# Performance work log

Hardware: AMD Instinct MI355X
Metric: run time of the kernel (lower is better)

Reference implementation:

```python
import jax, jax.numpy as jnp
import numpy as np

TOP_K = 8
ROUTED_SCALING_FACTOR = 1.0
EPS = 1e-20


def setup_inputs() -> dict:
    key = jax.random.key(0)
    k1, k2, k3 = jax.random.split(key, 3)
    T, D, E = 8192, 4096, 64
    x = jax.random.normal(k1, (T, D), dtype=jnp.float32)
    gate_weight = jax.random.normal(k2, (E, D), dtype=jnp.float32) * (1.0 / np.sqrt(D))
    bias = jax.random.normal(k3, (E,), dtype=jnp.float32) * 0.1
    return {"x": x, "gate_weight": gate_weight, "bias": bias}


def reference(x, gate_weight, bias):
    # logits: [T, E] = x [T, D] @ gate_weight.T [D, E]
    logits = jnp.einsum('td,ed->te', x.astype(jnp.float32), gate_weight)
    scores = jax.nn.sigmoid(logits)
    biased = scores + bias  # broadcast [E]
    # top-k on biased scores, sorted descending
    _, indices = jax.lax.top_k(biased, TOP_K)  # [T, K]
    selected_scores = jnp.take_along_axis(scores, indices, axis=-1)  # [T, K]
    normalized = selected_scores / (jnp.sum(selected_scores, axis=-1, keepdims=True) + EPS)
    weights = normalized * ROUTED_SCALING_FACTOR
    return (indices, weights)
```

## Files before the change

kernel.cpp:

```cpp
#include <hip/hip_runtime.h>
#include <math.h>
#include <stdint.h>

#define T_TOK 8192
#define DDIM  4096
#define NEXP  64
#define TOPK  8
#define MT    128
#define BK    32
#define RS    2048.0f

typedef __attribute__((ext_vector_type(8))) _Float16 half8;
typedef __attribute__((ext_vector_type(4))) float f32x4;
typedef __attribute__((address_space(3))) uint32_t lds_u32;
typedef const __attribute__((address_space(1))) uint32_t glb_u32;

__global__ __launch_bounds__(256) void pack_w(
    const float* __restrict__ gw, _Float16* __restrict__ wpk)
{
    const int g    = blockIdx.x * 256 + threadIdx.x;
    const int lane = g & 63;
    const int n    = (g >> 6) & 3;
    const int kt   = g >> 8;
    const int e    = n * 16 + (lane & 15);
    const int k    = kt * 32 + (lane >> 4) * 8;

    const float* src = gw + (size_t)e * DDIM + k;
    float4 v0 = *reinterpret_cast<const float4*>(src);
    float4 v1 = *reinterpret_cast<const float4*>(src + 4);
    const float v[8] = {v0.x, v0.y, v0.z, v0.w, v1.x, v1.y, v1.z, v1.w};

    half8 h0, h1;
    #pragma unroll
    for (int j = 0; j < 8; j++) {
        _Float16 a = (_Float16)v[j];
        h0[j] = a;
        h1[j] = (_Float16)((v[j] - (float)a) * RS);
    }
    _Float16* dst = wpk + (size_t)kt * 4096 + (size_t)(n * 2) * 512 + lane * 8;
    *reinterpret_cast<half8*>(dst)       = h0;
    *reinterpret_cast<half8*>(dst + 512) = h1;
}

template<int STEPS>
__global__ __launch_bounds__(512) void gemm_part(
    const float* __restrict__ x, const _Float16* __restrict__ wpk,
    float* __restrict__ part)
{
    __shared__ float    A[2][MT * BK];
    __shared__ _Float16 B[2][4096];

    const int tid  = threadIdx.x;
    const int lane = tid & 63;
    const int wv   = tid >> 6;
    const int wm   = wv & 3;
    const int wn   = wv >> 2;
    const int mt   = blockIdx.x & 63;
    const int slc  = blockIdx.x >> 6;
    const int m0   = mt * MT;
    const int kt0  = slc * STEPS;
    const int am   = lane & 15;
    const int ag   = lane >> 4;

    const int s_row0 = tid >> 3;
    const int s_c    = tid & 7;

#define STAGE(buf_, t_) do {                                                   \
        const size_t koff = (size_t)(kt0 + (t_)) * BK;                         \
        {                                       \
            int c0 = s_c ^ (s_row0 & 7);                                       \
            __builtin_amdgcn_global_load_lds(                                  \
                (glb_u32*)(x + (size_t)(m0 + s_row0) * DDIM + koff + c0 * 4),  \
                (lds_u32*)(&A[buf_][tid * 4]), 16, 0, 0);                      \
            int r1 = s_row0 + 64;                                              \
            int c1 = s_c ^ (r1 & 7);                                           \
            __builtin_amdgcn_global_load_lds(                                  \
                (glb_u32*)(x + (size_t)(m0 + r1) * DDIM + koff + c1 * 4),      \
                (lds_u32*)(&A[buf_][2048 + tid * 4]), 16, 0, 0);               \
        }                                                                      \
        {                                     \
            const _Float16* bs = wpk + (size_t)(kt0 + (t_)) * 4096 + tid * 8;  \
            __builtin_amdgcn_global_load_lds(                                  \
                (glb_u32*)bs, (lds_u32*)(&B[buf_][tid * 8]), 16, 0, 0);        \
        }                                                                      \
    } while (0)

    f32x4 aH[2][2], aM[2][2];
    #pragma unroll
    for (int f = 0; f < 2; f++)
        #pragma unroll
        for (int n = 0; n < 2; n++) {
            aH[f][n] = (f32x4){0.f, 0.f, 0.f, 0.f};
            aM[f][n] = (f32x4){0.f, 0.f, 0.f, 0.f};
        }

    STAGE(0, 0);
    __syncthreads();

    #pragma unroll 2
    for (int t = 0; t < STEPS; t++) {
        const int buf = t & 1;
        if (t + 1 < STEPS) STAGE(buf ^ 1, t + 1);

        half8 B0[2], B1[2];
        #pragma unroll
        for (int nf = 0; nf < 2; nf++) {
            const int nb = ((wn * 2 + nf) * 2) * 512 + lane * 8;
            B0[nf] = *reinterpret_cast<const half8*>(&B[buf][nb]);
            B1[nf] = *reinterpret_cast<const half8*>(&B[buf][nb + 512]);
        }

        #pragma unroll
        for (int f = 0; f < 2; f++) {
            const int row = wm * 32 + f * 16 + am;
            const int sw  = am & 7;
            float4 alo = *reinterpret_cast<const float4*>(
                &A[buf][row * BK + ((ag * 2 + 0) ^ sw) * 4]);
            float4 ahi = *reinterpret_cast<const float4*>(
                &A[buf][row * BK + ((ag * 2 + 1) ^ sw) * 4]);
            const float vv[8] = {alo.x, alo.y, alo.z, alo.w,
                                 ahi.x, ahi.y, ahi.z, ahi.w};
            half8 a0, a1;
            #pragma unroll
            for (int j = 0; j < 8; j++) {
                float v = vv[j];
                _Float16 h = (_Float16)v;
                a0[j] = h;
                a1[j] = (_Float16)((v - (float)h) * RS);
            }
            #pragma unroll
            for (int nf = 0; nf < 2; nf++) {
                aH[f][nf] = __builtin_amdgcn_mfma_f32_16x16x32_f16(a0, B0[nf], aH[f][nf], 0, 0, 0);
                aM[f][nf] = __builtin_amdgcn_mfma_f32_16x16x32_f16(a0, B1[nf], aM[f][nf], 0, 0, 0);
                aM[f][nf] = __builtin_amdgcn_mfma_f32_16x16x32_f16(a1, B0[nf], aM[f][nf], 0, 0, 0);
            }
        }
        __syncthreads();
    }
#undef STAGE

    const float i1 = 1.0f / RS;
    float* po = part + (size_t)slc * T_TOK * NEXP + (size_t)m0 * NEXP;
    #pragma unroll
    for (int f = 0; f < 2; f++)
        #pragma unroll
        for (int nf = 0; nf < 2; nf++)
            #pragma unroll
            for (int r = 0; r < 4; r++)
                po[(size_t)(wm * 32 + f * 16 + ag * 4 + r) * NEXP
                   + (wn * 2 + nf) * 16 + am]
                    = aH[f][nf][r] + aM[f][nf][r] * i1;
}

__global__ __launch_bounds__(256) void reduce_topk(
    const float* __restrict__ part, const float* __restrict__ bias,
    float* __restrict__ out, int S)
{
    const int wave = threadIdx.x >> 6;
    const int lane = threadIdx.x & 63;
    const int j    = blockIdx.x;
    const int g    = j & 7;
    const int q    = j >> 3;
    const int token = g * 128 + (q & 31) * 4 + (q >> 5) * 1024 + wave;
    if (token >= T_TOK) return;

    float logit = 0.f;
    for (int s = 0; s < S; s++)
        logit += part[(size_t)s * T_TOK * NEXP + (size_t)token * NEXP + lane];

    float score  = 1.f / (1.f + expf(-logit));
    float biased = score + bias[lane];

    float my_sc = 0.f;
    int   my_idx = 0;
    float ssum  = 0.f;

    #pragma unroll
    for (int jj = 0; jj < TOPK; jj++) {
        float v = biased;
        int   i = lane;
        #pragma unroll
        for (int off = 32; off >= 1; off >>= 1) {
            float ov = __shfl_xor(v, off);
            int   oi = __shfl_xor(i, off);
            if (ov > v || (ov == v && oi < i)) { v = ov; i = oi; }
        }
        float s_sel = __shfl(score, i);
        ssum += s_sel;
        if (lane == jj) { my_idx = i; my_sc = s_sel; }
        if (lane == i) biased = -INFINITY;
    }

    if (lane < TOPK) {
        out[(size_t)token * TOPK + lane] = (float)my_idx;
        out[(size_t)T_TOK * TOPK + (size_t)token * TOPK + lane]
            = my_sc / (ssum + 1e-20f);
    }
}

extern "C" void kernel_launch(void* const* d_in, const int* in_sizes, int n_in,
                              void* d_out, int out_size, void* d_ws, size_t ws_size,
                              hipStream_t stream) {
    (void)in_sizes; (void)n_in; (void)out_size;
    const float* x    = (const float*)d_in[0];
    const float* gw   = (const float*)d_in[1];
    const float* bias = (const float*)d_in[2];
    float* out = (float*)d_out;
    _Float16* wpk = (_Float16*)d_ws;
    float* part = (float*)(wpk + (size_t)DDIM * NEXP * 2);

    const size_t wpk_bytes = (size_t)DDIM * NEXP * 2 * sizeof(_Float16);
    const size_t per_slice = (size_t)T_TOK * NEXP * sizeof(float);
    int S = 1;
    for (int cand : {8, 4, 2}) {
        if (wpk_bytes + (size_t)cand * per_slice <= ws_size) { S = cand; break; }
    }

    pack_w<<<128, 256, 0, stream>>>(gw, wpk);

    dim3 b1(512);
    switch (S) {
        case 8: gemm_part<16><<<dim3(64 * 8), b1, 0, stream>>>(x, wpk, part); break;
        case 4: gemm_part<32><<<dim3(64 * 4), b1, 0, stream>>>(x, wpk, part); break;
        case 2: gemm_part<64><<<dim3(64 * 2), b1, 0, stream>>>(x, wpk, part); break;
        default: gemm_part<128><<<dim3(64), b1, 0, stream>>>(x, wpk, part); break;
    }

    reduce_topk<<<dim3(T_TOK / 4), 256, 0, stream>>>(part, bias, out, S);
}
```

Baseline: 47.99 us.

## Deepen GEMM pipeline to triple-buffered BK=64 stages and halve split-K

```diff
diff --git a/kernel.cpp b/kernel.cpp
--- a/kernel.cpp
+++ b/kernel.cpp
@@ -7,7 +7,7 @@
 #define NEXP  64
 #define TOPK  8
 #define MT    128
-#define BK    32
+#define BK    64
 #define RS    2048.0f
 
 typedef __attribute__((ext_vector_type(8))) _Float16 half8;
@@ -47,8 +47,8 @@
     const float* __restrict__ x, const _Float16* __restrict__ wpk,
     float* __restrict__ part)
 {
-    __shared__ float    A[2][MT * BK];
-    __shared__ _Float16 B[2][4096];
+    __shared__ float    A[3][MT * BK];
+    __shared__ _Float16 B[3][8192];
 
     const int tid  = threadIdx.x;
     const int lane = tid & 63;
@@ -58,30 +58,29 @@
     const int mt   = blockIdx.x & 63;
     const int slc  = blockIdx.x >> 6;
     const int m0   = mt * MT;
-    const int kt0  = slc * STEPS;
+    const int kt32 = slc * STEPS * 2;
     const int am   = lane & 15;
     const int ag   = lane >> 4;
 
-    const int s_row0 = tid >> 3;
-    const int s_c    = tid & 7;
-
 #define STAGE(buf_, t_) do {                                                   \
-        const size_t koff = (size_t)(kt0 + (t_)) * BK;                         \
-        {                                       \
-            int c0 = s_c ^ (s_row0 & 7);                                       \
+        const size_t koff = (size_t)(kt32 + 2 * (t_)) * 32;                    \
+        _Pragma("unroll")                                                      \
+        for (int r_ = 0; r_ < 4; r_++) {                                       \
+            int idx_ = r_ * 512 + tid;                                         \
+            int row_ = idx_ >> 4;                                              \
+            int c_   = idx_ & 15;                                              \
+            int cs_  = c_ ^ (row_ & 7);                                        \
             __builtin_amdgcn_global_load_lds(                                  \
-                (glb_u32*)(x + (size_t)(m0 + s_row0) * DDIM + koff + c0 * 4),  \
-                (lds_u32*)(&A[buf_][tid * 4]), 16, 0, 0);                      \
-            int r1 = s_row0 + 64;                                              \
-            int c1 = s_c ^ (r1 & 7);                                           \
+                (glb_u32*)(x + (size_t)(m0 + row_) * DDIM + koff + cs_ * 4),   \
+                (lds_u32*)(&A[buf_][idx_ * 4]), 16, 0, 0);                     \
+        }                                                                      \
+        const _Float16* bs_ = wpk + (size_t)(kt32 + 2 * (t_)) * 4096;          \
+        _Pragma("unroll")                                                      \
+        for (int r_ = 0; r_ < 2; r_++) {                                       \
+            int idx_ = r_ * 512 + tid;                                         \
             __builtin_amdgcn_global_load_lds(                                  \
-                (glb_u32*)(x + (size_t)(m0 + r1) * DDIM + koff + c1 * 4),      \
-                (lds_u32*)(&A[buf_][2048 + tid * 4]), 16, 0, 0);               \
-        }                                                                      \
-        {                                     \
-            const _Float16* bs = wpk + (size_t)(kt0 + (t_)) * 4096 + tid * 8;  \
-            __builtin_amdgcn_global_load_lds(                                  \
-                (glb_u32*)bs, (lds_u32*)(&B[buf_][tid * 8]), 16, 0, 0);        \
+                (glb_u32*)(bs_ + idx_ * 8),                                    \
+                (lds_u32*)(&B[buf_][idx_ * 8]), 16, 0, 0);                     \
         }                                                                      \
     } while (0)
 
@@ -95,47 +94,53 @@
         }
 
     STAGE(0, 0);
-    __syncthreads();
-
-    #pragma unroll 2
+    STAGE(1, 1);
+
     for (int t = 0; t < STEPS; t++) {
-        const int buf = t & 1;
-        if (t + 1 < STEPS) STAGE(buf ^ 1, t + 1);
-
-        half8 B0[2], B1[2];
-        #pragma unroll
-        for (int nf = 0; nf < 2; nf++) {
-            const int nb = ((wn * 2 + nf) * 2) * 512 + lane * 8;
-            B0[nf] = *reinterpret_cast<const half8*>(&B[buf][nb]);
-            B1[nf] = *reinterpret_cast<const half8*>(&B[buf][nb + 512]);
-        }
-
-        #pragma unroll
-        for (int f = 0; f < 2; f++) {
-            const int row = wm * 32 + f * 16 + am;
-            const int sw  = am & 7;
-            float4 alo = *reinterpret_cast<const float4*>(
-                &A[buf][row * BK + ((ag * 2 + 0) ^ sw) * 4]);
-            float4 ahi = *reinterpret_cast<const float4*>(
-                &A[buf][row * BK + ((ag * 2 + 1) ^ sw) * 4]);
-            const float vv[8] = {alo.x, alo.y, alo.z, alo.w,
-                                 ahi.x, ahi.y, ahi.z, ahi.w};
-            half8 a0, a1;
+        if (t + 1 < STEPS) asm volatile("s_waitcnt vmcnt(6)" ::: "memory");
+        else               asm volatile("s_waitcnt vmcnt(0)" ::: "memory");
+        __builtin_amdgcn_sched_barrier(0);
+        __builtin_amdgcn_s_barrier();
+        __builtin_amdgcn_sched_barrier(0);
+
+        if (t + 2 < STEPS) STAGE((t + 2) % 3, t + 2);
+
+        const int buf = t % 3;
+        #pragma unroll
+        for (int ktl = 0; ktl < 2; ktl++) {
+            half8 B0[2], B1[2];
             #pragma unroll
-            for (int j = 0; j < 8; j++) {
-                float v = vv[j];
-                _Float16 h = (_Float16)v;
-                a0[j] = h;
-                a1[j] = (_Float16)((v - (float)h) * RS);
+            for (int nf = 0; nf < 2; nf++) {
+                const int nb = ktl * 4096 + ((wn * 2 + nf) * 2) * 512 + lane * 8;
+                B0[nf] = *reinterpret_cast<const half8*>(&B[buf][nb]);
+                B1[nf] = *reinterpret_cast<const half8*>(&B[buf][nb + 512]);
             }
             #pragma unroll
-            for (int nf = 0; nf < 2; nf++) {
-                aH[f][nf] = __builtin_amdgcn_mfma_f32_16x16x32_f16(a0, B0[nf], aH[f][nf], 0, 0, 0);
-                aM[f][nf] = __builtin_amdgcn_mfma_f32_16x16x32_f16(a0, B1[nf], aM[f][nf], 0, 0, 0);
-                aM[f][nf] = __builtin_amdgcn_mfma_f32_16x16x32_f16(a1, B0[nf], aM[f][nf], 0, 0, 0);
+            for (int f = 0; f < 2; f++) {
+                const int row = wm * 32 + f * 16 + am;
+                const int sw  = row & 7;
+                const int s0  = (ktl * 8) | ((ag * 2 + 0) ^ sw);
+                const int s1  = (ktl * 8) | ((ag * 2 + 1) ^ sw);
+                float4 alo = *reinterpret_cast<const float4*>(&A[buf][row * BK + s0 * 4]);
+                float4 ahi = *reinterpret_cast<const float4*>(&A[buf][row * BK + s1 * 4]);
+                const float vv[8] = {alo.x, alo.y, alo.z, alo.w,
+                                     ahi.x, ahi.y, ahi.z, ahi.w};
+                half8 a0, a1;
+                #pragma unroll
+                for (int j = 0; j < 8; j++) {
+                    float v = vv[j];
+                    _Float16 h = (_Float16)v;
+                    a0[j] = h;
+                    a1[j] = (_Float16)((v - (float)h) * RS);
+                }
+                #pragma unroll
+                for (int nf = 0; nf < 2; nf++) {
+                    aH[f][nf] = __builtin_amdgcn_mfma_f32_16x16x32_f16(a0, B0[nf], aH[f][nf], 0, 0, 0);
+                    aM[f][nf] = __builtin_amdgcn_mfma_f32_16x16x32_f16(a0, B1[nf], aM[f][nf], 0, 0, 0);
+                    aM[f][nf] = __builtin_amdgcn_mfma_f32_16x16x32_f16(a1, B0[nf], aM[f][nf], 0, 0, 0);
+                }
             }
         }
-        __syncthreads();
     }
 #undef STAGE
 
@@ -212,7 +217,7 @@
     const size_t wpk_bytes = (size_t)DDIM * NEXP * 2 * sizeof(_Float16);
     const size_t per_slice = (size_t)T_TOK * NEXP * sizeof(float);
     int S = 1;
-    for (int cand : {8, 4, 2}) {
+    for (int cand : {4, 2}) {
         if (wpk_bytes + (size_t)cand * per_slice <= ws_size) { S = cand; break; }
     }
 
@@ -220,10 +225,9 @@
 
     dim3 b1(512);
     switch (S) {
-        case 8: gemm_part<16><<<dim3(64 * 8), b1, 0, stream>>>(x, wpk, part); break;
-        case 4: gemm_part<32><<<dim3(64 * 4), b1, 0, stream>>>(x, wpk, part); break;
-        case 2: gemm_part<64><<<dim3(64 * 2), b1, 0, stream>>>(x, wpk, part); break;
-        default: gemm_part<128><<<dim3(64), b1, 0, stream>>>(x, wpk, part); break;
+        case 4: gemm_part<16><<<dim3(64 * 4), b1, 0, stream>>>(x, wpk, part); break;
+        case 2: gemm_part<32><<<dim3(64 * 2), b1, 0, stream>>>(x, wpk, part); break;
+        default: gemm_part<64><<<dim3(64), b1, 0, stream>>>(x, wpk, part); break;
     }
 
     reduce_topk<<<dim3(T_TOK / 4), 256, 0, stream>>>(part, bias, out, S);
```

Measured after the change: 58.09 us. 21.1% more time.
